# Kernel optimization log

Hardware: AMD Instinct MI355X
Metric: run time of the kernel (lower is better)

Reference implementation:

```python
import jax, jax.numpy as jnp
import numpy as np

EPS = 1e-8  # torch.nn.CosineSimilarity default eps
N, D = 8192, 256


def setup_inputs() -> dict:
    key = jax.random.key(0)
    kq, kr = jax.random.split(key)
    query = jax.random.normal(kq, (N, D), dtype=jnp.float32)
    response = jax.random.normal(kr, (N, D), dtype=jnp.float32)
    return {"query": query, "response": response}


def reference(query, response):
    # cosine sim via one GEMM on raw vectors, normalized by clamped norm product
    # torch: x.y / max(||x||*||y||, eps)
    qn = jnp.linalg.norm(query, axis=-1)          # [N]
    rn = jnp.linalg.norm(response, axis=-1)       # [N]
    dots = query @ response.T                     # [N, N]
    denom = jnp.maximum(qn[:, None] * rn[None, :], EPS)
    all_score = dots / denom                      # [N, N] cosine sims
    pos_score = jnp.diagonal(all_score)           # [N]
    lse = jax.nn.logsumexp(all_score, axis=-1)    # [N]
    loss = jnp.sum(pos_score - lse)
    return -loss
```

## Files before the change

kernel.cpp:

```cpp
#include <hip/hip_runtime.h>
#include <hip/hip_bf16.h>

#define DDIM   256
#define BROWS  256
#define BN      64
#define NT       4
#define TS   (BN * DDIM)
#define SQRT_LOG2E 1.2011224087864498f

typedef float f32x4 __attribute__((ext_vector_type(4)));
typedef int   i32x4 __attribute__((ext_vector_type(4)));
typedef int   i32x8 __attribute__((ext_vector_type(8)));

__device__ __forceinline__ float exp2_hw(float x) {
  return __builtin_amdgcn_exp2f(x);
}

__device__ __forceinline__ f32x4 mfma_mx(i32x8 a, i32x8 b, f32x4 c) {
  return __builtin_amdgcn_mfma_scale_f32_16x16x128_f8f6f4(
      a, b, c, 0, 0, 0, 0x7F7F7F7F, 0, 0x7F7F7F7F);
}

__device__ __forceinline__ i32x8 cat8(i32x4 lo, i32x4 hi) {
  return __builtin_shufflevector(lo, hi, 0, 1, 2, 3, 4, 5, 6, 7);
}

__device__ __forceinline__ unsigned int pack4_fp8(float a0, float a1, float a2, float a3) {
  int v = __builtin_amdgcn_cvt_pk_fp8_f32(a0, a1, 0, false);
  v = __builtin_amdgcn_cvt_pk_fp8_f32(a2, a3, v, true);
  return (unsigned int)v;
}

__global__ __launch_bounds__(256) void prep_kernel(
    const float* __restrict__ q, const float* __restrict__ r,
    unsigned char* __restrict__ qf8, unsigned char* __restrict__ rf8,
    float* __restrict__ pos, float* __restrict__ row_sum,
    float* __restrict__ out) {
  if (blockIdx.x == 0 && threadIdx.x == 0) out[0] = 0.0f;
  int lane = threadIdx.x & 63, wave = threadIdx.x >> 6;
  int row = blockIdx.x * 4 + wave;
  size_t base = (size_t)row * DDIM + lane * 4;
  float4 qv = *(const float4*)(q + base);
  float4 rv = *(const float4*)(r + base);
  float qq = qv.x*qv.x + qv.y*qv.y + qv.z*qv.z + qv.w*qv.w;
  float rr = rv.x*rv.x + rv.y*rv.y + rv.z*rv.z + rv.w*rv.w;
  float qr = qv.x*rv.x + qv.y*rv.y + qv.z*rv.z + qv.w*rv.w;
  #pragma unroll
  for (int m = 1; m < 64; m <<= 1) {
    qq += __shfl_xor(qq, m);
    rr += __shfl_xor(rr, m);
    qr += __shfl_xor(qr, m);
  }
  float iq0 = 1.0f / sqrtf(qq);
  float ir0 = 1.0f / sqrtf(rr);
  float iq = iq0 * SQRT_LOG2E;
  float ir = ir0 * SQRT_LOG2E;
  unsigned int qp = pack4_fp8(qv.x*iq, qv.y*iq, qv.z*iq, qv.w*iq);
  unsigned int rp = pack4_fp8(rv.x*ir, rv.y*ir, rv.z*ir, rv.w*ir);
  *(unsigned int*)(qf8 + base) = qp;
  *(unsigned int*)(rf8 + base) = rp;
  if (lane == 0) {
    pos[row] = qr * iq0 * ir0;
    row_sum[row] = 0.0f;
  }
}

__device__ __forceinline__ void stage_quarter(char* dstBase,
                                              const unsigned char* src_base,
                                              int col0, int q, int tid) {
  int ch = q * 256 + tid;
  int c   = ch & 15;
  int g   = (ch >> 4) & 3;
  int pc  = (ch >> 6) & 1;
  int h   = (ch >> 7) & 1;
  int cf  = (ch >> 8) & 1;
  int p   = (ch >> 9) & 1;
  int col = p * 32 + cf * 16 + c;
  int src = col * 256 + h * 128 + g * 32 + pc * 16;
  __builtin_amdgcn_global_load_lds(
      (const __attribute__((address_space(1))) void*)((const char*)src_base + (size_t)col0 * 256 + src),
      (__attribute__((address_space(3))) void*)(dstBase + ch * 16),
      16, 0, 0);
}

__global__ __launch_bounds__(256, 2) void gemm_lse_kernel(
    const unsigned char* __restrict__ qf8, const unsigned char* __restrict__ rf8,
    float* __restrict__ row_sum) {
  __shared__ __attribute__((aligned(16))) unsigned char Bl[3 * TS];

  const int tid  = threadIdx.x;
  const int lane = tid & 63;
  const int wid  = tid >> 6;
  const int g = lane >> 4, c = lane & 15;
  const int row0  = blockIdx.x * BROWS;
  const int col00 = blockIdx.y * (NT * BN);
  const unsigned char* Rb = rf8;

  i32x8 av[4][2];
  const char* Ab = (const char*)qf8;
  #pragma unroll
  for (int m = 0; m < 4; ++m) {
    size_t rb0 = (size_t)(row0 + wid * 64 + m * 16 + c) * 256;
    #pragma unroll
    for (int h = 0; h < 2; ++h) {
      const char* p = Ab + rb0 + h * 128 + g * 32;
      av[m][h] = cat8(*(const i32x4*)(p), *(const i32x4*)(p + 16));
    }
  }
  #pragma unroll
  for (int q = 0; q < 4; ++q) stage_quarter((char*)Bl,      Rb, col00,      q, tid);
  #pragma unroll
  for (int q = 0; q < 4; ++q) stage_quarter((char*)Bl + TS, Rb, col00 + BN, q, tid);

  float rs[16];
  #pragma unroll
  for (int k = 0; k < 16; ++k) rs[k] = 0.0f;

  asm volatile("s_waitcnt vmcnt(4)" ::: "memory");
  __builtin_amdgcn_s_barrier();

  int rb = 0;
  int wb = 2 * TS;
  #pragma unroll 1
  for (int t = 0; t < NT; ++t) {
    const char* lbase = (const char*)Bl + rb + lane * 16;
    int scol = col00 + (t + 2) * BN;
    #pragma unroll
    for (int p = 0; p < 2; ++p) {
      stage_quarter((char*)Bl + wb, Rb, scol, 2 * p,     tid);
      stage_quarter((char*)Bl + wb, Rb, scol, 2 * p + 1, tid);

      i32x8 bv[2][2];
      #pragma unroll
      for (int cf = 0; cf < 2; ++cf)
        #pragma unroll
        for (int h = 0; h < 2; ++h) {
          const int off = (p * 8 + cf * 4 + h * 2) * 1024;
          bv[cf][h] = cat8(*(const i32x4*)(lbase + off),
                           *(const i32x4*)(lbase + off + 1024));
        }

      f32x4 acc[4][2];
      const f32x4 zero = {0.f, 0.f, 0.f, 0.f};
      #pragma unroll
      for (int m = 0; m < 4; ++m) { acc[m][0] = zero; acc[m][1] = zero; }
      __builtin_amdgcn_s_setprio(1);
      #pragma unroll
      for (int m = 0; m < 4; ++m)
        #pragma unroll
        for (int cf = 0; cf < 2; ++cf) {
          acc[m][cf] = mfma_mx(av[m][0], bv[cf][0], acc[m][cf]);
          acc[m][cf] = mfma_mx(av[m][1], bv[cf][1], acc[m][cf]);
        }
      __builtin_amdgcn_s_setprio(0);

      #pragma unroll
      for (int m = 0; m < 4; ++m)
        #pragma unroll
        for (int jj = 0; jj < 4; ++jj)
          rs[m * 4 + jj] += exp2_hw(acc[m][0][jj]) + exp2_hw(acc[m][1][jj]);
    }

    asm volatile("s_waitcnt vmcnt(4)" ::: "memory");
    __builtin_amdgcn_s_barrier();

    rb += TS; if (rb == 3 * TS) rb = 0;
    wb += TS; if (wb == 3 * TS) wb = 0;
  }

  asm volatile("s_waitcnt vmcnt(0)" ::: "memory");

  #pragma unroll
  for (int k = 0; k < 16; ++k) {
    float v = rs[k];
    v += __shfl_xor(v, 1);
    v += __shfl_xor(v, 2);
    v += __shfl_xor(v, 4);
    v += __shfl_xor(v, 8);
    if (c == 0) {
      int row = row0 + wid * 64 + (k >> 2) * 16 + g * 4 + (k & 3);
      atomicAdd(&row_sum[row], v);
    }
  }
}

__global__ __launch_bounds__(256) void finalize_kernel(
    const float* __restrict__ row_sum, const float* __restrict__ pos,
    float* __restrict__ out) {
  int i = blockIdx.x * 256 + threadIdx.x;
  float s = __logf(row_sum[i]) - pos[i];
  #pragma unroll
  for (int m = 1; m < 64; m <<= 1) s += __shfl_xor(s, m);
  __shared__ float red[4];
  if ((threadIdx.x & 63) == 0) red[threadIdx.x >> 6] = s;
  __syncthreads();
  if (threadIdx.x == 0)
    atomicAdd(out, red[0] + red[1] + red[2] + red[3]);
}

extern "C" void kernel_launch(void* const* d_in, const int* in_sizes, int n_in,
                              void* d_out, int out_size, void* d_ws, size_t ws_size,
                              hipStream_t stream) {
  const float* q = (const float*)d_in[0];
  const float* r = (const float*)d_in[1];
  int n = in_sizes[0] / DDIM;

  char* w = (char*)d_ws;
  size_t f8Bytes = (size_t)n * DDIM;
  unsigned char* qf8 = (unsigned char*)w;
  unsigned char* rf8 = (unsigned char*)(w + f8Bytes);
  float* pos     = (float*)(w + 2 * f8Bytes);
  float* row_sum = pos + n;

  prep_kernel<<<n / 4, 256, 0, stream>>>(q, r, qf8, rf8, pos, row_sum,
                                         (float*)d_out);

  dim3 grid(n / BROWS, n / (NT * BN));
  gemm_lse_kernel<<<grid, 256, 0, stream>>>(qf8, rf8, row_sum);

  finalize_kernel<<<n / 256, 256, 0, stream>>>(row_sum, pos, (float*)d_out);
}
```

Baseline: 38.88 us.

## Load B fragments directly from global memory, dropping LDS triple-buffer staging

Removes the LDS triple-buffered async staging of the response tile and its barriers, and has each wave load its B fragments for MFMA straight from global memory through L1/L2. It eliminates LDS traffic and block-wide synchronization, and frees shared memory so occupancy can rise. In exchange, all four waves redundantly fetch the same B data from cache, and there is no explicit prefetch to hide global load latency.

Measured after the change: 52.34 us. +34.6%, slower.

```diff
diff --git a/kernel.cpp b/kernel.cpp
--- a/kernel.cpp
+++ b/kernel.cpp
@@ -3,9 +3,7 @@
 
 #define DDIM   256
 #define BROWS  256
-#define BN      64
-#define NT       4
-#define TS   (BN * DDIM)
+#define BCH    256
 #define SQRT_LOG2E 1.2011224087864498f
 
 typedef float f32x4 __attribute__((ext_vector_type(4)));
@@ -65,36 +63,15 @@
   }
 }
 
-__device__ __forceinline__ void stage_quarter(char* dstBase,
-                                              const unsigned char* src_base,
-                                              int col0, int q, int tid) {
-  int ch = q * 256 + tid;
-  int c   = ch & 15;
-  int g   = (ch >> 4) & 3;
-  int pc  = (ch >> 6) & 1;
-  int h   = (ch >> 7) & 1;
-  int cf  = (ch >> 8) & 1;
-  int p   = (ch >> 9) & 1;
-  int col = p * 32 + cf * 16 + c;
-  int src = col * 256 + h * 128 + g * 32 + pc * 16;
-  __builtin_amdgcn_global_load_lds(
-      (const __attribute__((address_space(1))) void*)((const char*)src_base + (size_t)col0 * 256 + src),
-      (__attribute__((address_space(3))) void*)(dstBase + ch * 16),
-      16, 0, 0);
-}
-
 __global__ __launch_bounds__(256, 2) void gemm_lse_kernel(
     const unsigned char* __restrict__ qf8, const unsigned char* __restrict__ rf8,
     float* __restrict__ row_sum) {
-  __shared__ __attribute__((aligned(16))) unsigned char Bl[3 * TS];
-
   const int tid  = threadIdx.x;
   const int lane = tid & 63;
   const int wid  = tid >> 6;
   const int g = lane >> 4, c = lane & 15;
   const int row0  = blockIdx.x * BROWS;
-  const int col00 = blockIdx.y * (NT * BN);
-  const unsigned char* Rb = rf8;
+  const int col00 = blockIdx.y * BCH;
 
   i32x8 av[4][2];
   const char* Ab = (const char*)qf8;
@@ -107,68 +84,46 @@
       av[m][h] = cat8(*(const i32x4*)(p), *(const i32x4*)(p + 16));
     }
   }
-  #pragma unroll
-  for (int q = 0; q < 4; ++q) stage_quarter((char*)Bl,      Rb, col00,      q, tid);
-  #pragma unroll
-  for (int q = 0; q < 4; ++q) stage_quarter((char*)Bl + TS, Rb, col00 + BN, q, tid);
+
+  const char* b0 = (const char*)rf8 + (size_t)(col00 + c) * 256 + g * 32;
 
   float rs[16];
   #pragma unroll
   for (int k = 0; k < 16; ++k) rs[k] = 0.0f;
 
-  asm volatile("s_waitcnt vmcnt(4)" ::: "memory");
-  __builtin_amdgcn_s_barrier();
+  #pragma unroll 1
+  for (int p = 0; p < BCH / 32; ++p) {
+    const char* bp = b0 + p * 32 * 256;
 
-  int rb = 0;
-  int wb = 2 * TS;
-  #pragma unroll 1
-  for (int t = 0; t < NT; ++t) {
-    const char* lbase = (const char*)Bl + rb + lane * 16;
-    int scol = col00 + (t + 2) * BN;
+    i32x8 bv[2][2];
     #pragma unroll
-    for (int p = 0; p < 2; ++p) {
-      stage_quarter((char*)Bl + wb, Rb, scol, 2 * p,     tid);
-      stage_quarter((char*)Bl + wb, Rb, scol, 2 * p + 1, tid);
+    for (int cf = 0; cf < 2; ++cf)
+      #pragma unroll
+      for (int h = 0; h < 2; ++h) {
+        const char* a = bp + cf * 16 * 256 + h * 128;
+        bv[cf][h] = cat8(*(const i32x4*)(a), *(const i32x4*)(a + 16));
+      }
 
-      i32x8 bv[2][2];
+    f32x4 acc[4][2];
+    const f32x4 zero = {0.f, 0.f, 0.f, 0.f};
+    #pragma unroll
+    for (int m = 0; m < 4; ++m) { acc[m][0] = zero; acc[m][1] = zero; }
+    __builtin_amdgcn_s_setprio(1);
+    #pragma unroll
+    for (int m = 0; m < 4; ++m)
       #pragma unroll
-      for (int cf = 0; cf < 2; ++cf)
-        #pragma unroll
-        for (int h = 0; h < 2; ++h) {
-          const int off = (p * 8 + cf * 4 + h * 2) * 1024;
-          bv[cf][h] = cat8(*(const i32x4*)(lbase + off),
-                           *(const i32x4*)(lbase + off + 1024));
-        }
+      for (int cf = 0; cf < 2; ++cf) {
+        acc[m][cf] = mfma_mx(av[m][0], bv[cf][0], acc[m][cf]);
+        acc[m][cf] = mfma_mx(av[m][1], bv[cf][1], acc[m][cf]);
+      }
+    __builtin_amdgcn_s_setprio(0);
 
-      f32x4 acc[4][2];
-      const f32x4 zero = {0.f, 0.f, 0.f, 0.f};
+    #pragma unroll
+    for (int m = 0; m < 4; ++m)
       #pragma unroll
-      for (int m = 0; m < 4; ++m) { acc[m][0] = zero; acc[m][1] = zero; }
-      __builtin_amdgcn_s_setprio(1);
-      #pragma unroll
-      for (int m = 0; m < 4; ++m)
-        #pragma unroll
-        for (int cf = 0; cf < 2; ++cf) {
-          acc[m][cf] = mfma_mx(av[m][0], bv[cf][0], acc[m][cf]);
-          acc[m][cf] = mfma_mx(av[m][1], bv[cf][1], acc[m][cf]);
-        }
-      __builtin_amdgcn_s_setprio(0);
-
-      #pragma unroll
-      for (int m = 0; m < 4; ++m)
-        #pragma unroll
-        for (int jj = 0; jj < 4; ++jj)
-          rs[m * 4 + jj] += exp2_hw(acc[m][0][jj]) + exp2_hw(acc[m][1][jj]);
-    }
-
-    asm volatile("s_waitcnt vmcnt(4)" ::: "memory");
-    __builtin_amdgcn_s_barrier();
-
-    rb += TS; if (rb == 3 * TS) rb = 0;
-    wb += TS; if (wb == 3 * TS) wb = 0;
+      for (int jj = 0; jj < 4; ++jj)
+        rs[m * 4 + jj] += exp2_hw(acc[m][0][jj]) + exp2_hw(acc[m][1][jj]);
   }
-
-  asm volatile("s_waitcnt vmcnt(0)" ::: "memory");
 
   #pragma unroll
   for (int k = 0; k < 16; ++k) {
@@ -215,7 +170,7 @@
   prep_kernel<<<n / 4, 256, 0, stream>>>(q, r, qf8, rf8, pos, row_sum,
                                          (float*)d_out);
 
-  dim3 grid(n / BROWS, n / (NT * BN));
+  dim3 grid(n / BROWS, n / BCH);
   gemm_lse_kernel<<<grid, 256, 0, stream>>>(qf8, rf8, row_sum);
 
   finalize_kernel<<<n / 256, 256, 0, stream>>>(row_sum, pos, (float*)d_out);
```
